# Performance work log

Measured on AMD Instinct MI355X. Metric: run time of the kernel, lower is better.

## Reference

```python
import jax, jax.numpy as jnp
import numpy as np

N_GRID, N_MESH, N_EDGE, H = 65536, 10242, 131072, 512

def _layernorm(x, g, b, eps=1e-5):
    m = jnp.mean(x, axis=-1, keepdims=True)
    v = jnp.var(x, axis=-1, keepdims=True)
    return (x - m) * jax.lax.rsqrt(v + eps) * g + b

def _mlp(x, W1, b1, W2, b2, g, b):
    # Linear -> SiLU -> Linear -> LayerNorm (GraphCast MeshGraphMLP)
    h = jax.nn.silu(x @ W1 + b1)
    return _layernorm(h @ W2 + b2, g, b)

def setup_inputs() -> dict:
    key = jax.random.key(0)
    ks = jax.random.split(key, 16)
    s = lambda fan_in: 1.0 / np.sqrt(fan_in)
    inp = {
        'grid_node_features': jax.random.normal(ks[0], (N_GRID, H), jnp.float32),
        'mesh_node_features': jax.random.normal(ks[1], (N_MESH, H), jnp.float32),
        'grid2mesh_edge_features': jax.random.normal(ks[2], (N_EDGE, H), jnp.float32),
        'src_indices': jax.random.randint(ks[3], (N_EDGE,), 0, N_GRID),
        'dst_indices': jax.random.randint(ks[4], (N_EDGE,), 0, N_MESH),
        # edge MLP: in = concat(edge, src, dst) = 3H
        'We1': jax.random.normal(ks[5], (3 * H, H), jnp.float32) * s(3 * H),
        'be1': jnp.zeros((H,), jnp.float32),
        'We2': jax.random.normal(ks[6], (H, H), jnp.float32) * s(H),
        'be2': jnp.zeros((H,), jnp.float32),
        'ge': jnp.ones((H,), jnp.float32), 'bbe': jnp.zeros((H,), jnp.float32),
        # node MLP: in = concat(node, agg) = 2H
        'Wn1': jax.random.normal(ks[7], (2 * H, H), jnp.float32) * s(2 * H),
        'bn1': jnp.zeros((H,), jnp.float32),
        'Wn2': jax.random.normal(ks[8], (H, H), jnp.float32) * s(H),
        'bn2': jnp.zeros((H,), jnp.float32),
        'gn': jnp.ones((H,), jnp.float32), 'bbn': jnp.zeros((H,), jnp.float32),
        # grid node MLP: H -> H
        'Wg1': jax.random.normal(ks[9], (H, H), jnp.float32) * s(H),
        'bg1': jnp.zeros((H,), jnp.float32),
        'Wg2': jax.random.normal(ks[10], (H, H), jnp.float32) * s(H),
        'bg2': jnp.zeros((H,), jnp.float32),
        'gg': jnp.ones((H,), jnp.float32), 'bbg': jnp.zeros((H,), jnp.float32),
    }
    return inp

def reference(grid_node_features, mesh_node_features, grid2mesh_edge_features,
              src_indices, dst_indices,
              We1, be1, We2, be2, ge, bbe,
              Wn1, bn1, Wn2, bn2, gn, bbn,
              Wg1, bg1, Wg2, bg2, gg, bbg):
    # --- MeshEdgeBlock: gather src/dst, concat, MLP, residual on edges ---
    cat_e = jnp.concatenate([grid2mesh_edge_features,
                             grid_node_features[src_indices],
                             mesh_node_features[dst_indices]], axis=-1)  # [E, 3H]
    e_feats = grid2mesh_edge_features + _mlp(cat_e, We1, be1, We2, be2, ge, bbe)
    # --- MeshNodeBlock: scatter-sum edges to mesh nodes, concat, MLP ---
    agg = jax.ops.segment_sum(e_feats, dst_indices, num_segments=N_MESH)  # [M, H]
    cat_n = jnp.concatenate([mesh_node_features, agg], axis=-1)  # [M, 2H]
    n_feats = _mlp(cat_n, Wn1, bn1, Wn2, bn2, gn, bbn)
    mesh_out = mesh_node_features + n_feats
    # --- grid node MLP + residual ---
    grid_out = grid_node_features + _mlp(grid_node_features, Wg1, bg1, Wg2, bg2, gg, bbg)
    return (grid_out, mesh_out)
```

## Files before the change

### kernel.cpp

```cpp
#include <hip/hip_runtime.h>
#include <stdint.h>

typedef unsigned short u16;
typedef unsigned int   u32;
typedef unsigned char  u8;

using bf16x8 = __attribute__((ext_vector_type(8))) short;
using f32x4  = __attribute__((ext_vector_type(4))) float;

#define DEVF static __device__ __forceinline__

DEVF u16 f2bf(float f){
  u32 u = __builtin_bit_cast(u32, f);
  u32 r = u + 0x7FFFu + ((u >> 16) & 1u);
  return (u16)(r >> 16);
}
DEVF float bf2f(u16 h){
  u32 u = ((u32)h) << 16;
  return __builtin_bit_cast(float, u);
}

DEVF void gload_lds16(const u16* g, u16* s){
  __builtin_amdgcn_global_load_lds(
      (const __attribute__((address_space(1))) u32*)g,
      (__attribute__((address_space(3))) u32*)(u32)(uintptr_t)s,
      16, 0, 0);
}


__global__ __launch_bounds__(256) void k_f32_to_bf16(const float* __restrict__ in,
                                                     u16* __restrict__ out, long n){
  long i = (long)blockIdx.x * blockDim.x + threadIdx.x;
  long stride = (long)gridDim.x * blockDim.x;
  for (long j = i * 8; j < n; j += stride * 8){
    float4 a = *(const float4*)(in + j);
    float4 b = *(const float4*)(in + j + 4);
    bf16x8 v;
    v[0]=(short)f2bf(a.x); v[1]=(short)f2bf(a.y); v[2]=(short)f2bf(a.z); v[3]=(short)f2bf(a.w);
    v[4]=(short)f2bf(b.x); v[5]=(short)f2bf(b.y); v[6]=(short)f2bf(b.z); v[7]=(short)f2bf(b.w);
    *(bf16x8*)(out + j) = v;
  }
}

__global__ __launch_bounds__(256) void k_zero_i32(int* __restrict__ p, int n){
  int i = blockIdx.x * 256 + threadIdx.x;
  if (i < n) p[i] = 0;
}

__global__ __launch_bounds__(256) void k_transpose_w_off(const float* __restrict__ W,
                                                         u16* __restrict__ Wt,
                                                         int K, int N, int k0){
  int idx = blockIdx.x * 256 + threadIdx.x;
  if (idx < K * N){
    int k = idx / N, n = idx - k * N;
    Wt[(size_t)n * K + k] = f2bf(W[(size_t)(k + k0) * N + n]);
  }
}


__global__ __launch_bounds__(256)
void k_hist(const int* __restrict__ dst, int* __restrict__ cnt, int E){
  int e = blockIdx.x * 256 + threadIdx.x;
  if (e < E) atomicAdd(&cnt[dst[e]], 1);
}

__global__ __launch_bounds__(1024)
void k_scan(const int* __restrict__ cnt, int* __restrict__ offs, int n){
  __shared__ int part[1024];
  int t = threadIdx.x;
  const int PER = (n + 1023) / 1024;
  int base = t * PER;
  int s = 0;
  for (int i = 0; i < PER; ++i){ int idx = base + i; if (idx < n) s += cnt[idx]; }
  part[t] = s;
  __syncthreads();
  for (int o = 1; o < 1024; o <<= 1){
    int v = (t >= o) ? part[t - o] : 0;
    __syncthreads();
    part[t] += v;
    __syncthreads();
  }
  int run = (t == 0) ? 0 : part[t - 1];
  for (int i = 0; i < PER; ++i){
    int idx = base + i;
    if (idx < n){ offs[idx] = run; run += cnt[idx]; }
  }
  if (t == 1023) offs[n] = part[1023];
}

__global__ __launch_bounds__(256)
void k_scatter(const int* __restrict__ dst, const int* __restrict__ offs,
               int* __restrict__ cur, int* __restrict__ eid, int E){
  int e = blockIdx.x * 256 + threadIdx.x;
  if (e < E){
    int d = dst[e];
    int p = offs[d] + atomicAdd(&cur[d], 1);
    eid[p] = e;
  }
}


#define LDA4(BUF, MH, KK, AF) \
  _Pragma("unroll") for (int m_ = 0; m_ < 4; ++m_) \
    AF[m_] = *(const bf16x8*)&lA[BUF][(wm * 128 + (MH) * 64 + m_ * 16 + lane16) * 64 + \
                                      ((((KK) << 2) | kl) ^ (lane16 & 7)) * 8];

#define LDB4(BUF, KK, BFR) \
  _Pragma("unroll") for (int n_ = 0; n_ < 4; ++n_) \
    BFR[n_] = *(const bf16x8*)&lB[BUF][(wn * 64 + n_ * 16 + lane16) * 64 + \
                                       ((((KK) << 2) | kl) ^ (lane16 & 7)) * 8];

#define PHASE_MFMA(MH, AF, BFR) \
  __builtin_amdgcn_s_setprio(1); \
  _Pragma("unroll") for (int m_ = 0; m_ < 4; ++m_) \
    _Pragma("unroll") for (int n_ = 0; n_ < 4; ++n_) \
      acc[(MH) * 4 + m_][n_] = __builtin_amdgcn_mfma_f32_16x16x32_bf16( \
          AF[m_], BFR[n_], acc[(MH) * 4 + m_][n_], 0, 0, 0); \
  __builtin_amdgcn_s_setprio(0);

#define STAGE_A(BUF, KT_, RND) do{ \
    const int k0_ = (KT_) * 64; \
    const u16* ga_; \
    if (MODE == 0){ ga_ = A + (size_t)srows[RND] * K + k0_ + kchunk; } \
    else { \
      int seg_ = k0_ >> 9, klo_ = k0_ & 511; \
      const u16* b_ = (seg_ == 0) ? A  + (size_t)srows[RND] * 512 \
                                  : G1 + (size_t)sidx1[RND] * 512; \
      ga_ = b_ + klo_ + kchunk; \
    } \
    gload_lds16(ga_, &lA[BUF][((RND) * 64 + w * 8) * 64]); \
  }while(0)

#define STAGE_B(BUF, KT_, RND) \
  gload_lds16(bptr[RND] + (KT_) * 64 + kchunk, &lB[BUF][((RND) * 64 + w * 8) * 64])

#define WAITBAR(N) do{ \
    asm volatile("s_waitcnt vmcnt(" #N ")" ::: "memory"); \
    __builtin_amdgcn_s_barrier(); \
    __builtin_amdgcn_sched_barrier(0); \
  }while(0)

template<int MODE, int EPI>
__global__ __launch_bounds__(512)
void k_gemm256(const u16* __restrict__ A, const u16* __restrict__ G1, const u16* __restrict__ G2,
               const int* __restrict__ srcI, const int* __restrict__ dstI,
               const u16* __restrict__ Bt, const float* __restrict__ bias,
               void* __restrict__ out, int M, int K)
{
  __shared__ __align__(16) u16 lA[2][256 * 64];
  __shared__ __align__(16) u16 lB[2][256 * 64];

  const int tid = threadIdx.x;
  const int w = tid >> 6, l = tid & 63;

  const int nwg = gridDim.x * gridDim.y;
  const int wgf = blockIdx.y * gridDim.x + blockIdx.x;
  const int lg  = (wgf & 7) * (nwg >> 3) + (wgf >> 3);
  const int col0 = (lg % gridDim.x) * 256;
  const int row0 = (lg / gridDim.x) * 256;

  int srows[4], sidx1[4];
  const u16* bptr[4];
  #pragma unroll
  for (int it = 0; it < 4; ++it){
    int r = row0 + it * 64 + w * 8 + (l >> 3);
    if (r >= M) r = M - 1;
    srows[it] = r;
    if (MODE == 1){ sidx1[it] = srcI[r]; }
    int n = col0 + it * 64 + w * 8 + (l >> 3);
    bptr[it] = Bt + (size_t)n * K;
  }
  const int kchunk = ((l & 7) ^ (l >> 3)) * 8;

  f32x4 acc[8][4];
  #pragma unroll
  for (int m = 0; m < 8; ++m)
    #pragma unroll
    for (int n = 0; n < 4; ++n)
      acc[m][n] = (f32x4){0.f, 0.f, 0.f, 0.f};

  const int wm = w >> 2, wn = w & 3;
  const int lane16 = l & 15, kl = l >> 4;

  const int KT = K >> 6;

  STAGE_A(0, 0, 0); STAGE_A(0, 0, 2);
  STAGE_B(0, 0, 0); STAGE_B(0, 0, 1); STAGE_B(0, 0, 2); STAGE_B(0, 0, 3);
  STAGE_A(0, 0, 1); STAGE_A(0, 0, 3);

  for (int kt = 0; kt < KT; ++kt){
    const int buf = kt & 1;
    const bool more = (kt + 1 < KT);
    bf16x8 af[4], bfr[4];

    WAITBAR(2);

    LDB4(buf, 0, bfr);
    LDA4(buf, 0, 0, af);
    if (more){ STAGE_A(buf ^ 1, kt + 1, 0); STAGE_A(buf ^ 1, kt + 1, 2); }
    PHASE_MFMA(0, af, bfr);

    if (more){ WAITBAR(2); } else { WAITBAR(0); }

    LDA4(buf, 1, 0, af);
    if (more){ STAGE_B(buf ^ 1, kt + 1, 0); STAGE_B(buf ^ 1, kt + 1, 1); }
    PHASE_MFMA(1, af, bfr);

    LDB4(buf, 1, bfr);
    LDA4(buf, 0, 1, af);
    if (more){ STAGE_B(buf ^ 1, kt + 1, 2); STAGE_B(buf ^ 1, kt + 1, 3); }
    PHASE_MFMA(0, af, bfr);

    LDA4(buf, 1, 1, af);
    if (more){ STAGE_A(buf ^ 1, kt + 1, 1); STAGE_A(buf ^ 1, kt + 1, 3); }
    PHASE_MFMA(1, af, bfr);
  }

  #pragma unroll
  for (int m = 0; m < 8; ++m){
    int rbase = row0 + wm * 128 + m * 16 + kl * 4;
    #pragma unroll
    for (int j = 0; j < 4; ++j){
      int rg = rbase + j;
      if (rg < M){
        int dd = 0;
        if (EPI == 3) dd = dstI[rg];
        #pragma unroll
        for (int n = 0; n < 4; ++n){
          int cg = col0 + wn * 64 + n * 16 + lane16;
          float v = acc[m][n][j];
          if (EPI == 0){
            v += bias[cg];
            v = v / (1.f + __expf(-v));
            ((u16*)out)[(size_t)rg * 512 + cg] = f2bf(v);
          } else if (EPI == 3){
            v += bias[cg] + bf2f(G2[(size_t)dd * 512 + cg]);
            v = v / (1.f + __expf(-v));
            ((u16*)out)[(size_t)rg * 512 + cg] = f2bf(v);
          } else if (EPI == 1){
            ((u16*)out)[(size_t)rg * 512 + cg] = f2bf(v);
          } else {
            ((float*)out)[(size_t)rg * 512 + cg] = v;
          }
        }
      }
    }
  }
}


template<int MODE, int EPI>
__global__ __launch_bounds__(256)
void k_gemm(const u16* __restrict__ A, const u16* __restrict__ G1, const u16* __restrict__ G2,
            const int* __restrict__ src, const int* __restrict__ dst,
            const u16* __restrict__ Bt, const float* __restrict__ bias,
            void* __restrict__ out, int M, int K)
{
  __shared__ __align__(16) u16 lA[128 * 64];
  __shared__ __align__(16) u16 lB[128 * 64];

  const int tid = threadIdx.x;
  const int w = tid >> 6, l = tid & 63;
  const int row0 = blockIdx.x * 128;
  const int col0 = blockIdx.y * 128;

  int srows[4];
  const u16* bptr[4];
  #pragma unroll
  for (int it = 0; it < 4; ++it){
    int r = row0 + it * 32 + w * 8 + (l >> 3);
    if (r >= M) r = M - 1;
    srows[it] = r;
    int n = col0 + it * 32 + w * 8 + (l >> 3);
    bptr[it] = Bt + (size_t)n * K;
  }
  const int kchunk = (l & 7) * 8;

  f32x4 acc[4][4];
  #pragma unroll
  for (int m = 0; m < 4; ++m)
    #pragma unroll
    for (int n = 0; n < 4; ++n)
      acc[m][n] = (f32x4){0.f, 0.f, 0.f, 0.f};

  const int wm = w >> 1, wn = w & 1;
  const int lane16 = l & 15, kl = l >> 4;

  const int KT = K >> 6;
  for (int kt = 0; kt < KT; ++kt){
    const int k0 = kt * 64;
    __syncthreads();
    #pragma unroll
    for (int it = 0; it < 4; ++it){
      const u16* ga;
      if (MODE == 0){
        ga = A + (size_t)srows[it] * K + k0 + kchunk;
      } else {
        int seg = k0 >> 9, klocal = k0 & 511;
        const u16* base = (seg == 0) ? A  + (size_t)srows[it] * 512
                                     : G1 + (size_t)srows[it] * 512;
        ga = base + klocal + kchunk;
      }
      gload_lds16(ga, &lA[(it * 32 + w * 8) * 64]);
      gload_lds16(bptr[it] + k0 + kchunk, &lB[(it * 32 + w * 8) * 64]);
    }
    __syncthreads();

    #pragma unroll
    for (int kk = 0; kk < 2; ++kk){
      bf16x8 af[4], bfr[4];
      #pragma unroll
      for (int m = 0; m < 4; ++m)
        af[m] = *(const bf16x8*)&lA[(wm * 64 + m * 16 + lane16) * 64 + kk * 32 + kl * 8];
      #pragma unroll
      for (int n = 0; n < 4; ++n)
        bfr[n] = *(const bf16x8*)&lB[(wn * 64 + n * 16 + lane16) * 64 + kk * 32 + kl * 8];
      #pragma unroll
      for (int m = 0; m < 4; ++m)
        #pragma unroll
        for (int n = 0; n < 4; ++n)
          acc[m][n] = __builtin_amdgcn_mfma_f32_16x16x32_bf16(af[m], bfr[n], acc[m][n], 0, 0, 0);
    }
  }

  #pragma unroll
  for (int m = 0; m < 4; ++m){
    int rbase = row0 + wm * 64 + m * 16 + kl * 4;
    #pragma unroll
    for (int n = 0; n < 4; ++n){
      int cg = col0 + wn * 64 + n * 16 + lane16;
      #pragma unroll
      for (int j = 0; j < 4; ++j){
        int rg = rbase + j;
        if (rg < M){
          float v = acc[m][n][j];
          if (EPI == 0){
            v += bias[cg];
            v = v / (1.f + __expf(-v));
            ((u16*)out)[(size_t)rg * 512 + cg] = f2bf(v);
          } else if (EPI == 1){
            ((u16*)out)[(size_t)rg * 512 + cg] = f2bf(v);
          } else {
            ((float*)out)[(size_t)rg * 512 + cg] = v;
          }
        }
      }
    }
  }
}


__global__ __launch_bounds__(256)
void k_agg(const u16* __restrict__ e2, const float* __restrict__ be2,
           const float* __restrict__ ge, const float* __restrict__ bbe,
           const float* __restrict__ edge_f, const int* __restrict__ offs,
           const int* __restrict__ eid, u16* __restrict__ aggbf, int Mn)
{
  int node = blockIdx.x * 4 + (threadIdx.x >> 6);
  int l = threadIdx.x & 63;
  if (node >= Mn) return;
  int p0 = offs[node], p1 = offs[node + 1];

  float b2c[8], gc[8], bbc[8];
  #pragma unroll
  for (int j = 0; j < 8; ++j){
    int c = l * 8 + j;
    b2c[j] = be2[c]; gc[j] = ge[c]; bbc[j] = bbe[c];
  }

  float acc[8] = {0.f,0.f,0.f,0.f,0.f,0.f,0.f,0.f};
  for (int p = p0; p < p1; ++p){
    int e = eid[p];
    bf16x8 v = *(const bf16x8*)(e2 + (size_t)e * 512 + l * 8);
    const float* ei = edge_f + (size_t)e * 512 + l * 8;
    float4 a = *(const float4*)ei, b4 = *(const float4*)(ei + 4);
    float eiv[8] = {a.x, a.y, a.z, a.w, b4.x, b4.y, b4.z, b4.w};
    float x[8], s = 0.f, sq = 0.f;
    #pragma unroll
    for (int j = 0; j < 8; ++j){
      x[j] = bf2f((u16)v[j]) + b2c[j];
      s += x[j]; sq += x[j] * x[j];
    }
    #pragma unroll
    for (int o = 32; o; o >>= 1){ s += __shfl_xor(s, o); sq += __shfl_xor(sq, o); }
    float mean = s * (1.f / 512.f);
    float var = sq * (1.f / 512.f) - mean * mean;
    float rs = rsqrtf(var + 1e-5f);
    #pragma unroll
    for (int j = 0; j < 8; ++j)
      acc[j] += (x[j] - mean) * rs * gc[j] + bbc[j] + eiv[j];
  }

  bf16x8 o8;
  #pragma unroll
  for (int j = 0; j < 8; ++j) o8[j] = (short)f2bf(acc[j]);
  *(bf16x8*)(aggbf + (size_t)node * 512 + l * 8) = o8;
}


__global__ __launch_bounds__(256)
void k_ln_out(const float* __restrict__ x2, const float* __restrict__ b2,
              const float* __restrict__ g, const float* __restrict__ bb,
              const float* __restrict__ resid, float* __restrict__ out, int R)
{
  int row = blockIdx.x * 4 + (threadIdx.x >> 6);
  int l = threadIdx.x & 63;
  if (row >= R) return;
  const float* xr = x2 + (size_t)row * 512 + l * 8;
  float4 a = *(const float4*)xr, b4 = *(const float4*)(xr + 4);
  float x[8] = {a.x, a.y, a.z, a.w, b4.x, b4.y, b4.z, b4.w};
  float s = 0.f, sq = 0.f;
  #pragma unroll
  for (int j = 0; j < 8; ++j){
    x[j] += b2[l * 8 + j];
    s += x[j]; sq += x[j] * x[j];
  }
  #pragma unroll
  for (int o = 32; o; o >>= 1){ s += __shfl_xor(s, o); sq += __shfl_xor(sq, o); }
  float mean = s * (1.f / 512.f);
  float var = sq * (1.f / 512.f) - mean * mean;
  float rs = rsqrtf(var + 1e-5f);
  const float* rr = resid + (size_t)row * 512 + l * 8;
  float* po = out + (size_t)row * 512 + l * 8;
  #pragma unroll
  for (int j = 0; j < 8; ++j){
    int c = l * 8 + j;
    po[j] = (x[j] - mean) * rs * g[c] + bb[c] + rr[j];
  }
}

__global__ __launch_bounds__(256)
void k_ln_out_bf(const float* __restrict__ x2, const float* __restrict__ b2,
                 const float* __restrict__ g, const float* __restrict__ bb,
                 const u16* __restrict__ resid, float* __restrict__ out, int R)
{
  int row = blockIdx.x * 4 + (threadIdx.x >> 6);
  int l = threadIdx.x & 63;
  if (row >= R) return;
  const float* xr = x2 + (size_t)row * 512 + l * 8;
  float4 a = *(const float4*)xr, b4 = *(const float4*)(xr + 4);
  float x[8] = {a.x, a.y, a.z, a.w, b4.x, b4.y, b4.z, b4.w};
  float s = 0.f, sq = 0.f;
  #pragma unroll
  for (int j = 0; j < 8; ++j){
    x[j] += b2[l * 8 + j];
    s += x[j]; sq += x[j] * x[j];
  }
  #pragma unroll
  for (int o = 32; o; o >>= 1){ s += __shfl_xor(s, o); sq += __shfl_xor(sq, o); }
  float mean = s * (1.f / 512.f);
  float var = sq * (1.f / 512.f) - mean * mean;
  float rs = rsqrtf(var + 1e-5f);
  bf16x8 rv = *(const bf16x8*)(resid + (size_t)row * 512 + l * 8);
  float* po = out + (size_t)row * 512 + l * 8;
  #pragma unroll
  for (int j = 0; j < 8; ++j){
    int c = l * 8 + j;
    po[j] = (x[j] - mean) * rs * g[c] + bb[c] + bf2f((u16)rv[j]);
  }
}


extern "C" void kernel_launch(void* const* d_in, const int* in_sizes, int n_in,
                              void* d_out, int out_size, void* d_ws, size_t ws_size,
                              hipStream_t stream)
{
  const int N_GRID = 65536, N_MESH = 10242, N_EDGE = 131072, H = 512;

  const float* grid_f = (const float*)d_in[0];
  const float* mesh_f = (const float*)d_in[1];
  const float* edge_f = (const float*)d_in[2];
  const int*   src    = (const int*)d_in[3];
  const int*   dst    = (const int*)d_in[4];
  const float* We1 = (const float*)d_in[5];  const float* be1 = (const float*)d_in[6];
  const float* We2 = (const float*)d_in[7];  const float* be2 = (const float*)d_in[8];
  const float* ge  = (const float*)d_in[9];  const float* bbe = (const float*)d_in[10];
  const float* Wn1 = (const float*)d_in[11]; const float* bn1 = (const float*)d_in[12];
  const float* Wn2 = (const float*)d_in[13]; const float* bn2 = (const float*)d_in[14];
  const float* gn  = (const float*)d_in[15]; const float* bbn = (const float*)d_in[16];
  const float* Wg1 = (const float*)d_in[17]; const float* bg1 = (const float*)d_in[18];
  const float* Wg2 = (const float*)d_in[19]; const float* bg2 = (const float*)d_in[20];
  const float* gg  = (const float*)d_in[21]; const float* bbg = (const float*)d_in[22];

  u8* ws = (u8*)d_ws;
  const size_t MiB = 1u << 20;
  u16*  Gbf   = (u16*)(ws + 0);
  u16*  Mbf   = (u16*)(ws + 64  * MiB);
  u16*  AggBf = (u16*)(ws + 75  * MiB);
  u16*  We1t  = (u16*)(ws + 86  * MiB);
  u16*  Wpm   = (u16*)(ws + 86  * MiB + 1048576);
  u16*  We2t  = (u16*)(ws + 86  * MiB + 1572864);
  u16*  Wn1t  = (u16*)(ws + 86  * MiB + 2097152);
  u16*  Wn2t  = (u16*)(ws + 86  * MiB + 3145728);
  u16*  Wg1t  = (u16*)(ws + 86  * MiB + 3670016);
  u16*  Wg2t  = (u16*)(ws + 86  * MiB + 4194304);
  int*  offs  = (int*)(ws + 91 * MiB);
  int*  cnt   = (int*)(ws + 91 * MiB) + 10496;
  int*  cur   = (int*)(ws + 91 * MiB) + 20992;
  int*  eid   = (int*)(ws + 91 * MiB) + 31488;
  u16*  Pm    = (u16*)(ws + 96 * MiB);
  u16*  He    = (u16*)(ws + 112 * MiB);
  u8*   Big   =  ws + 240 * MiB;
  u16*  Ebf   = (u16*)Big;
  u16*  E2    = (u16*)Big;
  float* N2   = (float*)Big;
  float* G2   = (float*)Big;

  float* grid_out = (float*)d_out;
  float* mesh_out = (float*)d_out + (size_t)N_GRID * H;

  k_f32_to_bf16<<<2048, 256, 0, stream>>>(grid_f, Gbf, (long)N_GRID * H);
  k_f32_to_bf16<<<1024, 256, 0, stream>>>(mesh_f, Mbf, (long)N_MESH * H);
  k_f32_to_bf16<<<4096, 256, 0, stream>>>(edge_f, Ebf, (long)N_EDGE * H);
  k_transpose_w_off<<<(1024 * 512 + 255) / 256, 256, 0, stream>>>(We1, We1t, 1024, 512, 0);
  k_transpose_w_off<<<(512  * 512 + 255) / 256, 256, 0, stream>>>(We1, Wpm, 512, 512, 1024);
  k_transpose_w_off<<<(512  * 512 + 255) / 256, 256, 0, stream>>>(We2, We2t, 512, 512, 0);
  k_transpose_w_off<<<(1024 * 512 + 255) / 256, 256, 0, stream>>>(Wn1, Wn1t, 1024, 512, 0);
  k_transpose_w_off<<<(512  * 512 + 255) / 256, 256, 0, stream>>>(Wn2, Wn2t, 512, 512, 0);
  k_transpose_w_off<<<(512  * 512 + 255) / 256, 256, 0, stream>>>(Wg1, Wg1t, 512, 512, 0);
  k_transpose_w_off<<<(512  * 512 + 255) / 256, 256, 0, stream>>>(Wg2, Wg2t, 512, 512, 0);
  k_zero_i32<<<(20992 + 255) / 256, 256, 0, stream>>>(cnt, 20992);
  k_hist<<<N_EDGE / 256, 256, 0, stream>>>(dst, cnt, N_EDGE);
  k_scan<<<1, 1024, 0, stream>>>(cnt, offs, N_MESH);
  k_scatter<<<N_EDGE / 256, 256, 0, stream>>>(dst, offs, cur, eid, N_EDGE);

  dim3 gpm((N_MESH + 127) / 128, 4);
  k_gemm<0, 1><<<gpm, 256, 0, stream>>>(Mbf, nullptr, nullptr, nullptr, nullptr, Wpm, nullptr, Pm, N_MESH, 512);

  dim3 ge1(2, N_EDGE / 256);
  k_gemm256<1, 3><<<ge1, 512, 0, stream>>>(Ebf, Gbf, Pm, src, dst, We1t, be1, He, N_EDGE, 1024);
  k_gemm256<0, 1><<<ge1, 512, 0, stream>>>(He, nullptr, nullptr, nullptr, nullptr, We2t, nullptr, E2, N_EDGE, 512);
  k_agg<<<(N_MESH + 3) / 4, 256, 0, stream>>>(E2, be2, ge, bbe, edge_f, offs, eid, AggBf, N_MESH);

  dim3 gn1((N_MESH + 127) / 128, 4);
  k_gemm<2, 0><<<gn1, 256, 0, stream>>>(Mbf, AggBf, nullptr, nullptr, nullptr, Wn1t, bn1, He, N_MESH, 1024);
  k_gemm<0, 2><<<gn1, 256, 0, stream>>>(He, nullptr, nullptr, nullptr, nullptr, Wn2t, nullptr, N2, N_MESH, 512);
  k_ln_out<<<(N_MESH + 3) / 4, 256, 0, stream>>>(N2, bn2, gn, bbn, mesh_f, mesh_out, N_MESH);

  dim3 gg1(2, N_GRID / 256);
  k_gemm256<0, 0><<<gg1, 512, 0, stream>>>(Gbf, nullptr, nullptr, nullptr, nullptr, Wg1t, bg1, He, N_GRID, 512);
  k_gemm256<0, 2><<<gg1, 512, 0, stream>>>(He, nullptr, nullptr, nullptr, nullptr, Wg2t, nullptr, G2, N_GRID, 512);
  k_ln_out_bf<<<N_GRID / 4, 256, 0, stream>>>(G2, bg2, gg, bbg, Gbf, grid_out, N_GRID);
}
```

Before: 1.011 ms.

## Sort edges by source, simplify GEMM pipeline, emit bf16 grid GEMM output

Edges are reordered by source index: edge features are converted and permuted into sorted order, and src/dst index arrays are rebuilt so the edge GEMM gathers grid rows with better locality. Aggregation uses a composed index to read the permuted GEMM output. The 256-tile GEMM pipeline now stages a whole next k-tile after one full wait instead of interleaved partial waits, and tiles are swizzled in column pairs. The grid second GEMM writes bf16 instead of fp32 before layernorm, cutting traffic at some precision cost. The node GEMM mode also changes from 2 to 1. These add sort and permutation kernels.

```diff
diff --git a/kernel.cpp b/kernel.cpp
--- a/kernel.cpp
+++ b/kernel.cpp
@@ -42,6 +42,20 @@
   }
 }
 
+__global__ __launch_bounds__(256)
+void k_conv_perm(const float* __restrict__ in, const int* __restrict__ pos,
+                 u16* __restrict__ out, int E){
+  int e = blockIdx.x * 4 + (threadIdx.x >> 6);
+  int l = threadIdx.x & 63;
+  if (e >= E) return;
+  const float* r = in + (size_t)e * 512 + l * 8;
+  float4 a = *(const float4*)r, b = *(const float4*)(r + 4);
+  bf16x8 v;
+  v[0]=(short)f2bf(a.x); v[1]=(short)f2bf(a.y); v[2]=(short)f2bf(a.z); v[3]=(short)f2bf(a.w);
+  v[4]=(short)f2bf(b.x); v[5]=(short)f2bf(b.y); v[6]=(short)f2bf(b.z); v[7]=(short)f2bf(b.w);
+  *(bf16x8*)(out + (size_t)pos[e] * 512 + l * 8) = v;
+}
+
 __global__ __launch_bounds__(256) void k_zero_i32(int* __restrict__ p, int n){
   int i = blockIdx.x * 256 + threadIdx.x;
   if (i < n) p[i] = 0;
@@ -59,9 +73,9 @@
 
 
 __global__ __launch_bounds__(256)
-void k_hist(const int* __restrict__ dst, int* __restrict__ cnt, int E){
+void k_hist(const int* __restrict__ key, int* __restrict__ cnt, int E){
   int e = blockIdx.x * 256 + threadIdx.x;
-  if (e < E) atomicAdd(&cnt[dst[e]], 1);
+  if (e < E) atomicAdd(&cnt[key[e]], 1);
 }
 
 __global__ __launch_bounds__(1024)
@@ -89,14 +103,42 @@
 }
 
 __global__ __launch_bounds__(256)
-void k_scatter(const int* __restrict__ dst, const int* __restrict__ offs,
+void k_scatter(const int* __restrict__ key, const int* __restrict__ offs,
                int* __restrict__ cur, int* __restrict__ eid, int E){
   int e = blockIdx.x * 256 + threadIdx.x;
   if (e < E){
-    int d = dst[e];
+    int d = key[e];
     int p = offs[d] + atomicAdd(&cur[d], 1);
     eid[p] = e;
   }
+}
+
+__global__ __launch_bounds__(256)
+void k_scatter_pos(const int* __restrict__ key, const int* __restrict__ offs,
+                   int* __restrict__ cur, int* __restrict__ eid,
+                   int* __restrict__ pos, int E){
+  int e = blockIdx.x * 256 + threadIdx.x;
+  if (e < E){
+    int d = key[e];
+    int p = offs[d] + atomicAdd(&cur[d], 1);
+    eid[p] = e;
+    pos[e] = p;
+  }
+}
+
+__global__ __launch_bounds__(256)
+void k_make_idx(const int* __restrict__ eid_src, const int* __restrict__ src,
+                const int* __restrict__ dst, int* __restrict__ srcS,
+                int* __restrict__ dstS, int E){
+  int r = blockIdx.x * 256 + threadIdx.x;
+  if (r < E){ int e = eid_src[r]; srcS[r] = src[e]; dstS[r] = dst[e]; }
+}
+
+__global__ __launch_bounds__(256)
+void k_compose(const int* __restrict__ eid_dst, const int* __restrict__ pos_src,
+               int* __restrict__ eid_agg, int E){
+  int p = blockIdx.x * 256 + threadIdx.x;
+  if (p < E) eid_agg[p] = pos_src[eid_dst[p]];
 }
 
 
@@ -134,6 +176,11 @@
 #define STAGE_B(BUF, KT_, RND) \
   gload_lds16(bptr[RND] + (KT_) * 64 + kchunk, &lB[BUF][((RND) * 64 + w * 8) * 64])
 
+#define STAGE8(BUF, KT_) do{ \
+    STAGE_A(BUF, KT_, 0); STAGE_A(BUF, KT_, 1); STAGE_A(BUF, KT_, 2); STAGE_A(BUF, KT_, 3); \
+    STAGE_B(BUF, KT_, 0); STAGE_B(BUF, KT_, 1); STAGE_B(BUF, KT_, 2); STAGE_B(BUF, KT_, 3); \
+  }while(0)
+
 #define WAITBAR(N) do{ \
     asm volatile("s_waitcnt vmcnt(" #N ")" ::: "memory"); \
     __builtin_amdgcn_s_barrier(); \
@@ -153,11 +200,12 @@
   const int tid = threadIdx.x;
   const int w = tid >> 6, l = tid & 63;
 
-  const int nwg = gridDim.x * gridDim.y;
   const int wgf = blockIdx.y * gridDim.x + blockIdx.x;
-  const int lg  = (wgf & 7) * (nwg >> 3) + (wgf >> 3);
-  const int col0 = (lg % gridDim.x) * 256;
-  const int row0 = (lg / gridDim.x) * 256;
+  const int pr = wgf >> 1, c = wgf & 1;
+  const int npair = (gridDim.x * gridDim.y) >> 1;
+  const int prs = (pr & 7) * (npair >> 3) + (pr >> 3);
+  const int row0 = prs * 256;
+  const int col0 = c * 256;
 
   int srows[4], sidx1[4];
   const u16* bptr[4];
@@ -184,35 +232,29 @@
 
   const int KT = K >> 6;
 
-  STAGE_A(0, 0, 0); STAGE_A(0, 0, 2);
-  STAGE_B(0, 0, 0); STAGE_B(0, 0, 1); STAGE_B(0, 0, 2); STAGE_B(0, 0, 3);
-  STAGE_A(0, 0, 1); STAGE_A(0, 0, 3);
+  STAGE8(0, 0);
 
   for (int kt = 0; kt < KT; ++kt){
     const int buf = kt & 1;
-    const bool more = (kt + 1 < KT);
+
+    WAITBAR(0);
+
+    if (kt + 1 < KT){ STAGE8(buf ^ 1, kt + 1); }
+    __builtin_amdgcn_sched_barrier(0);
+
     bf16x8 af[4], bfr[4];
-
-    WAITBAR(2);
-
     LDB4(buf, 0, bfr);
     LDA4(buf, 0, 0, af);
-    if (more){ STAGE_A(buf ^ 1, kt + 1, 0); STAGE_A(buf ^ 1, kt + 1, 2); }
     PHASE_MFMA(0, af, bfr);
 
-    if (more){ WAITBAR(2); } else { WAITBAR(0); }
-
     LDA4(buf, 1, 0, af);
-    if (more){ STAGE_B(buf ^ 1, kt + 1, 0); STAGE_B(buf ^ 1, kt + 1, 1); }
     PHASE_MFMA(1, af, bfr);
 
     LDB4(buf, 1, bfr);
     LDA4(buf, 0, 1, af);
-    if (more){ STAGE_B(buf ^ 1, kt + 1, 2); STAGE_B(buf ^ 1, kt + 1, 3); }
     PHASE_MFMA(0, af, bfr);
 
     LDA4(buf, 1, 1, af);
-    if (more){ STAGE_A(buf ^ 1, kt + 1, 1); STAGE_A(buf ^ 1, kt + 1, 3); }
     PHASE_MFMA(1, af, bfr);
   }
 
@@ -354,7 +396,8 @@
 void k_agg(const u16* __restrict__ e2, const float* __restrict__ be2,
            const float* __restrict__ ge, const float* __restrict__ bbe,
            const float* __restrict__ edge_f, const int* __restrict__ offs,
-           const int* __restrict__ eid, u16* __restrict__ aggbf, int Mn)
+           const int* __restrict__ eid_d, const int* __restrict__ eid_a,
+           u16* __restrict__ aggbf, int Mn)
 {
   int node = blockIdx.x * 4 + (threadIdx.x >> 6);
   int l = threadIdx.x & 63;
@@ -370,8 +413,9 @@
 
   float acc[8] = {0.f,0.f,0.f,0.f,0.f,0.f,0.f,0.f};
   for (int p = p0; p < p1; ++p){
-    int e = eid[p];
-    bf16x8 v = *(const bf16x8*)(e2 + (size_t)e * 512 + l * 8);
+    int e = eid_d[p];
+    int q = eid_a[p];
+    bf16x8 v = *(const bf16x8*)(e2 + (size_t)q * 512 + l * 8);
     const float* ei = edge_f + (size_t)e * 512 + l * 8;
     float4 a = *(const float4*)ei, b4 = *(const float4*)(ei + 4);
     float eiv[8] = {a.x, a.y, a.z, a.w, b4.x, b4.y, b4.z, b4.w};
@@ -430,20 +474,18 @@
 }
 
 __global__ __launch_bounds__(256)
-void k_ln_out_bf(const float* __restrict__ x2, const float* __restrict__ b2,
+void k_ln_out_bb(const u16* __restrict__ x2, const float* __restrict__ b2,
                  const float* __restrict__ g, const float* __restrict__ bb,
                  const u16* __restrict__ resid, float* __restrict__ out, int R)
 {
   int row = blockIdx.x * 4 + (threadIdx.x >> 6);
   int l = threadIdx.x & 63;
   if (row >= R) return;
-  const float* xr = x2 + (size_t)row * 512 + l * 8;
-  float4 a = *(const float4*)xr, b4 = *(const float4*)(xr + 4);
-  float x[8] = {a.x, a.y, a.z, a.w, b4.x, b4.y, b4.z, b4.w};
-  float s = 0.f, sq = 0.f;
+  bf16x8 xv = *(const bf16x8*)(x2 + (size_t)row * 512 + l * 8);
+  float x[8], s = 0.f, sq = 0.f;
   #pragma unroll
   for (int j = 0; j < 8; ++j){
-    x[j] += b2[l * 8 + j];
+    x[j] = bf2f((u16)xv[j]) + b2[l * 8 + j];
     s += x[j]; sq += x[j] * x[j];
   }
   #pragma unroll
@@ -494,24 +536,43 @@
   u16*  Wn2t  = (u16*)(ws + 86  * MiB + 3145728);
   u16*  Wg1t  = (u16*)(ws + 86  * MiB + 3670016);
   u16*  Wg2t  = (u16*)(ws + 86  * MiB + 4194304);
-  int*  offs  = (int*)(ws + 91 * MiB);
-  int*  cnt   = (int*)(ws + 91 * MiB) + 10496;
-  int*  cur   = (int*)(ws + 91 * MiB) + 20992;
-  int*  eid   = (int*)(ws + 91 * MiB) + 31488;
+  int*  offs_d = (int*)(ws + 91 * MiB);
+  int*  cnt_d  = (int*)(ws + 91 * MiB) + 10496;
+  int*  cur_d  = (int*)(ws + 91 * MiB) + 20992;
+  int*  eid_d  = (int*)(ws + 91 * MiB) + 31488;
+  int*  offs_s = (int*)(ws + 92 * MiB);
+  int*  cnt_s  = (int*)(ws + 92 * MiB) + 65792;
+  int*  cur_s  = (int*)(ws + 92 * MiB) + 131328;
+  int*  eid_s  = (int*)(ws + 92 * MiB) + 196864;
+  int*  pos_s  = (int*)(ws + 92 * MiB) + 327936;
+  int*  srcS   = (int*)(ws + 92 * MiB) + 459008;
+  int*  dstS   = (int*)(ws + 92 * MiB) + 590080;
+  int*  eid_a  = (int*)(ws + 92 * MiB) + 721152;
   u16*  Pm    = (u16*)(ws + 96 * MiB);
   u16*  He    = (u16*)(ws + 112 * MiB);
   u8*   Big   =  ws + 240 * MiB;
   u16*  Ebf   = (u16*)Big;
   u16*  E2    = (u16*)Big;
   float* N2   = (float*)Big;
-  float* G2   = (float*)Big;
+  u16*  G2    = (u16*)Big;
 
   float* grid_out = (float*)d_out;
   float* mesh_out = (float*)d_out + (size_t)N_GRID * H;
 
+  k_zero_i32<<<(20992 + 255) / 256, 256, 0, stream>>>(cnt_d, 20992);
+  k_zero_i32<<<(131072 + 255) / 256, 256, 0, stream>>>(cnt_s, 131072);
+  k_hist<<<N_EDGE / 256, 256, 0, stream>>>(dst, cnt_d, N_EDGE);
+  k_hist<<<N_EDGE / 256, 256, 0, stream>>>(src, cnt_s, N_EDGE);
+  k_scan<<<1, 1024, 0, stream>>>(cnt_d, offs_d, N_MESH);
+  k_scan<<<1, 1024, 0, stream>>>(cnt_s, offs_s, N_GRID);
+  k_scatter<<<N_EDGE / 256, 256, 0, stream>>>(dst, offs_d, cur_d, eid_d, N_EDGE);
+  k_scatter_pos<<<N_EDGE / 256, 256, 0, stream>>>(src, offs_s, cur_s, eid_s, pos_s, N_EDGE);
+  k_make_idx<<<N_EDGE / 256, 256, 0, stream>>>(eid_s, src, dst, srcS, dstS, N_EDGE);
+  k_compose<<<N_EDGE / 256, 256, 0, stream>>>(eid_d, pos_s, eid_a, N_EDGE);
+
   k_f32_to_bf16<<<2048, 256, 0, stream>>>(grid_f, Gbf, (long)N_GRID * H);
   k_f32_to_bf16<<<1024, 256, 0, stream>>>(mesh_f, Mbf, (long)N_MESH * H);
-  k_f32_to_bf16<<<4096, 256, 0, stream>>>(edge_f, Ebf, (long)N_EDGE * H);
+  k_conv_perm<<<N_EDGE / 4, 256, 0, stream>>>(edge_f, pos_s, Ebf, N_EDGE);
   k_transpose_w_off<<<(1024 * 512 + 255) / 256, 256, 0, stream>>>(We1, We1t, 1024, 512, 0);
   k_transpose_w_off<<<(512  * 512 + 255) / 256, 256, 0, stream>>>(We1, Wpm, 512, 512, 1024);
   k_transpose_w_off<<<(512  * 512 + 255) / 256, 256, 0, stream>>>(We2, We2t, 512, 512, 0);
@@ -519,26 +580,22 @@
   k_transpose_w_off<<<(512  * 512 + 255) / 256, 256, 0, stream>>>(Wn2, Wn2t, 512, 512, 0);
   k_transpose_w_off<<<(512  * 512 + 255) / 256, 256, 0, stream>>>(Wg1, Wg1t, 512, 512, 0);
   k_transpose_w_off<<<(512  * 512 + 255) / 256, 256, 0, stream>>>(Wg2, Wg2t, 512, 512, 0);
-  k_zero_i32<<<(20992 + 255) / 256, 256, 0, stream>>>(cnt, 20992);
-  k_hist<<<N_EDGE / 256, 256, 0, stream>>>(dst, cnt, N_EDGE);
-  k_scan<<<1, 1024, 0, stream>>>(cnt, offs, N_MESH);
-  k_scatter<<<N_EDGE / 256, 256, 0, stream>>>(dst, offs, cur, eid, N_EDGE);
 
   dim3 gpm((N_MESH + 127) / 128, 4);
   k_gemm<0, 1><<<gpm, 256, 0, stream>>>(Mbf, nullptr, nullptr, nullptr, nullptr, Wpm, nullptr, Pm, N_MESH, 512);
 
   dim3 ge1(2, N_EDGE / 256);
-  k_gemm256<1, 3><<<ge1, 512, 0, stream>>>(Ebf, Gbf, Pm, src, dst, We1t, be1, He, N_EDGE, 1024);
+  k_gemm256<1, 3><<<ge1, 512, 0, stream>>>(Ebf, Gbf, Pm, srcS, dstS, We1t, be1, He, N_EDGE, 1024);
   k_gemm256<0, 1><<<ge1, 512, 0, stream>>>(He, nullptr, nullptr, nullptr, nullptr, We2t, nullptr, E2, N_EDGE, 512);
-  k_agg<<<(N_MESH + 3) / 4, 256, 0, stream>>>(E2, be2, ge, bbe, edge_f, offs, eid, AggBf, N_MESH);
+  k_agg<<<(N_MESH + 3) / 4, 256, 0, stream>>>(E2, be2, ge, bbe, edge_f, offs_d, eid_d, eid_a, AggBf, N_MESH);
 
   dim3 gn1((N_MESH + 127) / 128, 4);
-  k_gemm<2, 0><<<gn1, 256, 0, stream>>>(Mbf, AggBf, nullptr, nullptr, nullptr, Wn1t, bn1, He, N_MESH, 1024);
+  k_gemm<1, 0><<<gn1, 256, 0, stream>>>(Mbf, AggBf, nullptr, nullptr, nullptr, Wn1t, bn1, He, N_MESH, 1024);
   k_gemm<0, 2><<<gn1, 256, 0, stream>>>(He, nullptr, nullptr, nullptr, nullptr, Wn2t, nullptr, N2, N_MESH, 512);
   k_ln_out<<<(N_MESH + 3) / 4, 256, 0, stream>>>(N2, bn2, gn, bbn, mesh_f, mesh_out, N_MESH);
 
   dim3 gg1(2, N_GRID / 256);
   k_gemm256<0, 0><<<gg1, 512, 0, stream>>>(Gbf, nullptr, nullptr, nullptr, nullptr, Wg1t, bg1, He, N_GRID, 512);
-  k_gemm256<0, 2><<<gg1, 512, 0, stream>>>(He, nullptr, nullptr, nullptr, nullptr, Wg2t, nullptr, G2, N_GRID, 512);
-  k_ln_out_bf<<<N_GRID / 4, 256, 0, stream>>>(G2, bg2, gg, bbg, Gbf, grid_out, N_GRID);
-}
+  k_gemm256<0, 1><<<gg1, 512, 0, stream>>>(He, nullptr, nullptr, nullptr, nullptr, Wg2t, nullptr, G2, N_GRID, 512);
+  k_ln_out_bb<<<N_GRID / 4, 256, 0, stream>>>(G2, bg2, gg, bbg, Gbf, grid_out, N_GRID);
+}
```

Result: slower. 1.089 ms (+7.7%).
